# Optimization experiments

Hardware: AMD Instinct MI355X
Metric: run time of the kernel (lower is better)

## Reference

```python
import jax, jax.numpy as jnp
import numpy as np

N_BINS = 10


def setup_inputs() -> dict:
    key = jax.random.key(0)
    k1, k2 = jax.random.split(key)
    N, C = 1000000, 128
    logits = jax.random.normal(k1, (N, C), dtype=jnp.float32)
    labels = jax.random.randint(k2, (N,), 0, C, dtype=jnp.int64)
    return {"logits": logits, "labels": labels}


def reference(logits, labels):
    N = logits.shape[0]
    probs = jax.nn.softmax(logits, axis=1)
    confidences = jnp.max(probs, axis=1)          # [N]
    predictions = jnp.argmax(probs, axis=1)       # [N]
    accuracies = (predictions == labels).astype(jnp.float32)

    # Bin i covers (i/n, (i+1)/n]; ceil(conf*n)-1 gives that index.
    bin_idx = jnp.clip(
        jnp.ceil(confidences * N_BINS).astype(jnp.int32) - 1, 0, N_BINS - 1
    )

    counts = jax.ops.segment_sum(jnp.ones_like(confidences), bin_idx, num_segments=N_BINS)
    conf_sum = jax.ops.segment_sum(confidences, bin_idx, num_segments=N_BINS)
    acc_sum = jax.ops.segment_sum(accuracies, bin_idx, num_segments=N_BINS)

    prop_in_bin = counts / N
    nonempty = counts > 0
    denom = jnp.maximum(counts, 1.0)
    acc_in_bin = jnp.where(nonempty, acc_sum / denom, 0.0)
    conf_in_bin = jnp.where(nonempty, conf_sum / denom, 0.0)

    CE = conf_in_bin - acc_in_bin
    abs_CE = jnp.where(nonempty, jnp.abs(CE), 0.0)
    ece = jnp.sum(abs_CE * prop_in_bin)
    oe = jnp.sum(jnp.where(nonempty, conf_in_bin * jnp.maximum(CE, 0.0), 0.0) * prop_in_bin)

    # (ece, per-bin accuracy, oe, per-bin proportion, per-bin |CE|)
    return ece, acc_in_bin, oe, prop_in_bin, abs_CE
```

## Files before the change

kernel.cpp:

```cpp
#include <hip/hip_runtime.h>

#define N_BINS 10


__global__ void ece_zero_ws(unsigned int* ws) {
    int i = threadIdx.x;
    if (i < 3 * N_BINS) ws[i] = 0u;
}

__global__ __launch_bounds__(256) void ece_main(
        const float* __restrict__ logits,
        const int*   __restrict__ labels,
        float*       __restrict__ ws,
        int N) {
    __shared__ float        s_conf[N_BINS];
    __shared__ float        s_acc [N_BINS];
    __shared__ unsigned int s_cnt [N_BINS];
    if (threadIdx.x < N_BINS) {
        s_conf[threadIdx.x] = 0.f;
        s_acc [threadIdx.x] = 0.f;
        s_cnt [threadIdx.x] = 0u;
    }
    __syncthreads();

    const int lane32       = threadIdx.x & 31;
    const int rowInBlock   = threadIdx.x >> 5;
    const int rowsPerBlock = blockDim.x >> 5;

    long long row = (long long)blockIdx.x * rowsPerBlock + rowInBlock;
    const long long rowStride = (long long)gridDim.x * rowsPerBlock;

    for (; row < N; row += rowStride) {
        const float4* p = (const float4*)(logits + row * 128);
        float4 v = p[lane32];

        float m = v.x; int idx = lane32 * 4;
        if (v.y > m) { m = v.y; idx = lane32 * 4 + 1; }
        if (v.z > m) { m = v.z; idx = lane32 * 4 + 2; }
        if (v.w > m) { m = v.w; idx = lane32 * 4 + 3; }

        #pragma unroll
        for (int mask = 16; mask >= 1; mask >>= 1) {
            float om = __shfl_xor(m, mask);
            int   oi = __shfl_xor(idx, mask);
            if (om > m || (om == m && oi < idx)) { m = om; idx = oi; }
        }

        float s = __expf(v.x - m) + __expf(v.y - m) + __expf(v.z - m) + __expf(v.w - m);
        #pragma unroll
        for (int mask = 16; mask >= 1; mask >>= 1) s += __shfl_xor(s, mask);

        if (lane32 == 0) {
            float conf = 1.0f / s;
            int bin = (int)ceilf(conf * 10.0f) - 1;
            bin = min(max(bin, 0), N_BINS - 1);
            float acc = (labels[row] == idx) ? 1.0f : 0.0f;
            atomicAdd(&s_conf[bin], conf);
            atomicAdd(&s_acc [bin], acc);
            atomicAdd(&s_cnt [bin], 1u);
        }
    }

    __syncthreads();
    if (threadIdx.x < N_BINS) {
        atomicAdd(&ws[threadIdx.x],              s_conf[threadIdx.x]);
        atomicAdd(&ws[N_BINS + threadIdx.x],     s_acc [threadIdx.x]);
        atomicAdd((unsigned int*)ws + 2 * N_BINS + threadIdx.x, s_cnt[threadIdx.x]);
    }
}

__global__ void ece_finalize(const float* __restrict__ ws, float* __restrict__ out, int N) {
    if (threadIdx.x == 0 && blockIdx.x == 0) {
        float ece = 0.f, oe = 0.f;
        for (int b = 0; b < N_BINS; ++b) {
            float cs = ws[b];
            float as = ws[N_BINS + b];
            unsigned int c = ((const unsigned int*)ws)[2 * N_BINS + b];
            float cnt   = (float)c;
            float prop  = cnt / (float)N;
            float denom = fmaxf(cnt, 1.0f);
            bool  ne    = (c > 0);
            float acc_in  = ne ? as / denom : 0.f;
            float conf_in = ne ? cs / denom : 0.f;
            float CE    = conf_in - acc_in;
            float absCE = ne ? fabsf(CE) : 0.f;
            ece += absCE * prop;
            oe  += (ne ? conf_in * fmaxf(CE, 0.f) : 0.f) * prop;
            out[1 + b]  = acc_in;
            out[12 + b] = prop;
            out[22 + b] = absCE;
        }
        out[0]  = ece;
        out[11] = oe;
    }
}

extern "C" void kernel_launch(void* const* d_in, const int* in_sizes, int n_in,
                              void* d_out, int out_size, void* d_ws, size_t ws_size,
                              hipStream_t stream) {
    const float* logits = (const float*)d_in[0];
    const int*   labels = (const int*)d_in[1];
    float*       out    = (float*)d_out;
    float*       ws     = (float*)d_ws;
    const int N = in_sizes[1];

    hipLaunchKernelGGL(ece_zero_ws, dim3(1), dim3(64), 0, stream, (unsigned int*)ws);

    const int block = 256;
    const int rowsPerBlock = block / 32;
    int grid = (N + rowsPerBlock - 1) / rowsPerBlock;
    if (grid > 4096) grid = 4096;
    hipLaunchKernelGGL(ece_main, dim3(grid), dim3(block), 0, stream,
                       logits, labels, ws, N);

    hipLaunchKernelGGL(ece_finalize, dim3(1), dim3(64), 0, stream, ws, out, N);
}
```

Measured before the change: 714.2 us.

## Replace shuffle argmax with DPP half-wave reductions and label-value accuracy test

Drops the max-shift in softmax and computes exp(max)/sum(exp) directly. Row max, exp sum and the logit at the label index are reduced with DPP row/broadcast ops over each half-wave instead of shuffle loops, and accuracy becomes a comparison of the label's logit with the max rather than an argmax index match. Count and accuracy are packed into one 64-bit shared atomic, and the grid cap is halved. The unshifted exp can overflow for large logits, and the tie-breaking behaviour of the accuracy test differs from argmax.

```diff
diff --git a/kernel.cpp b/kernel.cpp
--- a/kernel.cpp
+++ b/kernel.cpp
@@ -2,10 +2,35 @@
 
 #define N_BINS 10
 
+template<int CTRL, bool BC>
+__device__ __forceinline__ float dpp_f(float x, float old_) {
+    int r = __builtin_amdgcn_update_dpp(__builtin_bit_cast(int, old_),
+                                        __builtin_bit_cast(int, x),
+                                        CTRL, 0xf, 0xf, BC);
+    return __builtin_bit_cast(float, r);
+}
+
+__device__ __forceinline__ float half_reduce_add(float x) {
+    x += dpp_f<0x111, true>(x, 0.f);
+    x += dpp_f<0x112, true>(x, 0.f);
+    x += dpp_f<0x114, true>(x, 0.f);
+    x += dpp_f<0x118, true>(x, 0.f);
+    x += dpp_f<0x142, true>(x, 0.f);
+    return x;
+}
+
+__device__ __forceinline__ float half_reduce_max(float x) {
+    x = fmaxf(x, dpp_f<0x111, false>(x, x));
+    x = fmaxf(x, dpp_f<0x112, false>(x, x));
+    x = fmaxf(x, dpp_f<0x114, false>(x, x));
+    x = fmaxf(x, dpp_f<0x118, false>(x, x));
+    x = fmaxf(x, dpp_f<0x142, false>(x, x));
+    return x;
+}
 
 __global__ void ece_zero_ws(unsigned int* ws) {
     int i = threadIdx.x;
-    if (i < 3 * N_BINS) ws[i] = 0u;
+    if (i < 64) ws[i] = 0u;
 }
 
 __global__ __launch_bounds__(256) void ece_main(
@@ -13,13 +38,11 @@
         const int*   __restrict__ labels,
         float*       __restrict__ ws,
         int N) {
-    __shared__ float        s_conf[N_BINS];
-    __shared__ float        s_acc [N_BINS];
-    __shared__ unsigned int s_cnt [N_BINS];
+    __shared__ float              s_conf[N_BINS];
+    __shared__ unsigned long long s_pack[N_BINS];
     if (threadIdx.x < N_BINS) {
         s_conf[threadIdx.x] = 0.f;
-        s_acc [threadIdx.x] = 0.f;
-        s_cnt [threadIdx.x] = 0u;
+        s_pack[threadIdx.x] = 0ull;
     }
     __syncthreads();
 
@@ -33,49 +56,46 @@
     for (; row < N; row += rowStride) {
         const float4* p = (const float4*)(logits + row * 128);
         float4 v = p[lane32];
+        int la = labels[row];
 
-        float m = v.x; int idx = lane32 * 4;
-        if (v.y > m) { m = v.y; idx = lane32 * 4 + 1; }
-        if (v.z > m) { m = v.z; idx = lane32 * 4 + 2; }
-        if (v.w > m) { m = v.w; idx = lane32 * 4 + 3; }
-
-        #pragma unroll
-        for (int mask = 16; mask >= 1; mask >>= 1) {
-            float om = __shfl_xor(m, mask);
-            int   oi = __shfl_xor(idx, mask);
-            if (om > m || (om == m && oi < idx)) { m = om; idx = oi; }
+        float m4 = fmaxf(fmaxf(v.x, v.y), fmaxf(v.z, v.w));
+        float e4 = __expf(v.x) + __expf(v.y) + __expf(v.z) + __expf(v.w);
+        float vl = 0.f;
+        if ((la >> 2) == lane32) {
+            int r = la & 3;
+            vl = (r == 0) ? v.x : (r == 1) ? v.y : (r == 2) ? v.z : v.w;
         }
 
-        float s = __expf(v.x - m) + __expf(v.y - m) + __expf(v.z - m) + __expf(v.w - m);
-        #pragma unroll
-        for (int mask = 16; mask >= 1; mask >>= 1) s += __shfl_xor(s, mask);
+        float S  = half_reduce_add(e4);
+        float M  = half_reduce_max(m4);
+        float VL = half_reduce_add(vl);
 
-        if (lane32 == 0) {
-            float conf = 1.0f / s;
+        if (lane32 == 31) {
+            float conf = __expf(M) / S;
             int bin = (int)ceilf(conf * 10.0f) - 1;
             bin = min(max(bin, 0), N_BINS - 1);
-            float acc = (labels[row] == idx) ? 1.0f : 0.0f;
+            unsigned long long packed = 0x100000000ull | (unsigned long long)(VL == M ? 1u : 0u);
             atomicAdd(&s_conf[bin], conf);
-            atomicAdd(&s_acc [bin], acc);
-            atomicAdd(&s_cnt [bin], 1u);
+            atomicAdd(&s_pack[bin], packed);
         }
     }
 
     __syncthreads();
     if (threadIdx.x < N_BINS) {
-        atomicAdd(&ws[threadIdx.x],              s_conf[threadIdx.x]);
-        atomicAdd(&ws[N_BINS + threadIdx.x],     s_acc [threadIdx.x]);
-        atomicAdd((unsigned int*)ws + 2 * N_BINS + threadIdx.x, s_cnt[threadIdx.x]);
+        atomicAdd(&ws[threadIdx.x], s_conf[threadIdx.x]);
+        atomicAdd((unsigned long long*)((char*)ws + 64) + threadIdx.x, s_pack[threadIdx.x]);
     }
 }
 
 __global__ void ece_finalize(const float* __restrict__ ws, float* __restrict__ out, int N) {
     if (threadIdx.x == 0 && blockIdx.x == 0) {
+        const unsigned long long* pack = (const unsigned long long*)((const char*)ws + 64);
         float ece = 0.f, oe = 0.f;
         for (int b = 0; b < N_BINS; ++b) {
             float cs = ws[b];
-            float as = ws[N_BINS + b];
-            unsigned int c = ((const unsigned int*)ws)[2 * N_BINS + b];
+            unsigned long long pk = pack[b];
+            unsigned int c  = (unsigned int)(pk >> 32);
+            float as        = (float)(unsigned int)(pk & 0xffffffffull);
             float cnt   = (float)c;
             float prop  = cnt / (float)N;
             float denom = fmaxf(cnt, 1.0f);
@@ -109,7 +129,7 @@
     const int block = 256;
     const int rowsPerBlock = block / 32;
     int grid = (N + rowsPerBlock - 1) / rowsPerBlock;
-    if (grid > 4096) grid = 4096;
+    if (grid > 2048) grid = 2048;
     hipLaunchKernelGGL(ece_main, dim3(grid), dim3(block), 0, stream,
                        logits, labels, ws, N);
 
```

Measured after the change: 654.6 us. -8.3%, faster.
